# Optimization experiments

Measured on AMD Instinct MI355X. Metric: run time of the kernel, lower is better.

## Reference

```python
import jax, jax.numpy as jnp
import numpy as np

B, T, S, D, H = 4, 8, 512, 1024, 16
HD = D // H  # head dim = 64
N_LATENTS = 16


def setup_inputs() -> dict:
    key = jax.random.key(0)
    ks = jax.random.split(key, 10)
    x = jax.random.normal(ks[0], (B, T, S, D), dtype=jnp.float32)
    modality_ids = jax.random.randint(ks[1], (S,), 0, 8, dtype=jnp.int32)
    init = 0.02
    wq = jax.random.normal(ks[2], (D, H, HD), dtype=jnp.float32) * init
    wk = jax.random.normal(ks[3], (D, H, HD), dtype=jnp.float32) * init
    wv = jax.random.normal(ks[4], (D, H, HD), dtype=jnp.float32) * init
    wo = jax.random.normal(ks[5], (H, HD, D), dtype=jnp.float32) * init
    bq = jnp.zeros((H, HD), dtype=jnp.float32)
    bk = jnp.zeros((H, HD), dtype=jnp.float32)
    bv = jnp.zeros((H, HD), dtype=jnp.float32)
    bo = jnp.zeros((D,), dtype=jnp.float32)
    return {"x": x, "modality_ids": modality_ids, "wq": wq, "bq": bq,
            "wk": wk, "bk": bk, "wv": wv, "bv": bv, "wo": wo, "bo": bo}


def _encoder_mask(modality_ids, n_latents):
    # mask[q, k] = True means query q may attend to key k.
    # encoder mode: latent queries (index < n_latents) attend to everything,
    # non-latent queries attend only to same-modality keys.
    S_ = modality_ids.shape[0]
    is_q_lat = (jnp.arange(S_) < n_latents)[:, None]          # [S,1]
    same_mod = modality_ids[:, None] == modality_ids[None, :]  # [S,S]
    return jnp.where(is_q_lat, True, same_mod)                 # [S,S] bool


def reference(x, modality_ids, wq, bq, wk, bk, wv, bv, wo, bo):
    mask = _encoder_mask(modality_ids, N_LATENTS)  # [S,S]
    # QKV projections (flax DenseGeneral D -> (H, HD), with bias)
    q = jnp.einsum('btsd,dhc->btshc', x, wq) + bq
    k = jnp.einsum('btsd,dhc->btshc', x, wk) + bk
    v = jnp.einsum('btsd,dhc->btshc', x, wv) + bv
    # flax scales the query by 1/sqrt(head_dim) before the dot product
    q = q / jnp.sqrt(jnp.asarray(HD, dtype=q.dtype))
    scores = jnp.einsum('btqhc,btkhc->bthqk', q, k)  # [B,T,H,S,S]
    big_neg = jnp.finfo(scores.dtype).min
    scores = jnp.where(mask[None, None, None, :, :], scores, big_neg)
    attn = jax.nn.softmax(scores, axis=-1)
    out = jnp.einsum('bthqk,btkhc->btqhc', attn, v)  # [B,T,S,H,HD]
    y = jnp.einsum('btqhc,hcd->btqd', out, wo) + bo  # [B,T,S,D]
    return y
```

## Files before the change

### kernel.cpp

```cpp
#include <hip/hip_runtime.h>
#include <hip/hip_bf16.h>


typedef __attribute__((ext_vector_type(8))) short bf16x8;
typedef __attribute__((ext_vector_type(4))) float f32x4;
typedef __attribute__((ext_vector_type(16))) float f32x16;
typedef __attribute__((ext_vector_type(4))) unsigned short u16x4;
typedef __attribute__((ext_vector_type(2))) unsigned uint32x2;
typedef __attribute__((ext_vector_type(4))) unsigned uint32x4;

static __device__ __forceinline__ short f2bs(float f) {
  __hip_bfloat16 h = __float2bfloat16(f);
  return __builtin_bit_cast(short, h);
}

static __device__ __forceinline__ unsigned pack2bf(float a, float b) {
  return (unsigned)(unsigned short)f2bs(a) | ((unsigned)(unsigned short)f2bs(b) << 16);
}

static __device__ __forceinline__ void gload16(const void* g, void* l) {
  __builtin_amdgcn_global_load_lds(
      (const __attribute__((address_space(1))) void*)g,
      (__attribute__((address_space(3))) void*)l, 16, 0, 0);
}

__global__ __launch_bounds__(256) void cvt_x_kernel(const float* __restrict__ in,
                                                    __hip_bfloat16* __restrict__ out) {
  int i = blockIdx.x * 256 + threadIdx.x;
  const float4* p = (const float4*)in;
  float4 a = p[2 * i], b = p[2 * i + 1];
  bf16x8 v;
  v[0] = f2bs(a.x); v[1] = f2bs(a.y); v[2] = f2bs(a.z); v[3] = f2bs(a.w);
  v[4] = f2bs(b.x); v[5] = f2bs(b.y); v[6] = f2bs(b.z); v[7] = f2bs(b.w);
  *(bf16x8*)(out + (size_t)i * 8) = v;
}

__global__ __launch_bounds__(256) void trans_w_kernel(const float* __restrict__ in,
                                                      __hip_bfloat16* __restrict__ out) {
  __shared__ float tile[64][65];
  const int R0 = blockIdx.y * 64, C0 = blockIdx.x * 64;
  const int c = threadIdx.x & 63, r4 = threadIdx.x >> 6;
#pragma unroll
  for (int i = 0; i < 16; ++i) {
    int r = r4 * 16 + i;
    tile[r][c] = in[(size_t)(R0 + r) * 1024 + C0 + c];
  }
  __syncthreads();
#pragma unroll
  for (int i = 0; i < 16; ++i) {
    int r = r4 * 16 + i;
    out[(size_t)(C0 + r) * 1024 + R0 + c] = __float2bfloat16(tile[c][r]);
  }
}

template <int EPI>
__global__ __launch_bounds__(256) void gemm_bt(
    const __hip_bfloat16* __restrict__ A, const __hip_bfloat16* __restrict__ Bt,
    const float* __restrict__ bias0, const float* __restrict__ bias1,
    const float* __restrict__ bias2, __hip_bfloat16* __restrict__ o0,
    __hip_bfloat16* __restrict__ o1, __hip_bfloat16* __restrict__ o2,
    float* __restrict__ yout) {
  __shared__ __hip_bfloat16 Asm[128 * 64];
  __shared__ __hip_bfloat16 Bsm[128 * 64];
  const int tid = threadIdx.x;
  const int w = tid >> 6, lane = tid & 63;
  const int g = lane >> 4, l15 = lane & 15;
  const int wm = w >> 1, wn = w & 1;
  const long M0 = (long)blockIdx.y * 128, N0 = (long)blockIdx.x * 128;
  const int srow = lane >> 3;
  const int skk = (lane & 7) * 8;

  f32x4 acc[4][4];
  const f32x4 fz = {0.f, 0.f, 0.f, 0.f};
#pragma unroll
  for (int i = 0; i < 4; ++i)
#pragma unroll
    for (int j = 0; j < 4; ++j) acc[i][j] = fz;

  for (int kt = 0; kt < 16; ++kt) {
    const int k0 = kt * 64;
    __syncthreads();
#pragma unroll
    for (int i = 0; i < 4; ++i) {
      const int chunk = w * 4 + i;
      const int row = chunk * 8 + srow;
      gload16(A + (M0 + row) * 1024 + k0 + skk, Asm + chunk * 512);
      gload16(Bt + (N0 + row) * 1024 + k0 + skk, Bsm + chunk * 512);
    }
    __syncthreads();
#pragma unroll
    for (int ks = 0; ks < 2; ++ks) {
      bf16x8 af[4], bfr[4];
#pragma unroll
      for (int mt = 0; mt < 4; ++mt)
        af[mt] = *(const bf16x8*)(Asm + (wm * 64 + mt * 16 + l15) * 64 + ks * 32 + g * 8);
#pragma unroll
      for (int nt = 0; nt < 4; ++nt)
        bfr[nt] = *(const bf16x8*)(Bsm + (wn * 64 + nt * 16 + l15) * 64 + ks * 32 + g * 8);
#pragma unroll
      for (int mt = 0; mt < 4; ++mt)
#pragma unroll
        for (int nt = 0; nt < 4; ++nt)
          acc[mt][nt] = __builtin_amdgcn_mfma_f32_16x16x32_bf16(af[mt], bfr[nt],
                                                                acc[mt][nt], 0, 0, 0);
    }
  }

  const int mb = (int)M0 + wm * 64;
  const int nb = (int)N0 + wn * 64;
#pragma unroll
  for (int mt = 0; mt < 4; ++mt) {
    const int m0r = mb + mt * 16 + g * 4;
    const int bt_ = m0r >> 9, s0 = m0r & 511;
#pragma unroll
    for (int nt = 0; nt < 4; ++nt) {
      const int n = nb + nt * 16 + l15;
      f32x4 v = acc[mt][nt];
      if (EPI == 0) {
        const int t = n >> 10, r = n & 1023;
        const int h = r >> 6, c = r & 63;
        if (t == 0) {
          const float b = bias0[r];
          size_t base = (((size_t)bt_ * 16 + h) * 512 + s0) * 64 + c;
#pragma unroll
          for (int j = 0; j < 4; ++j)
            o0[base + (size_t)j * 64] = __float2bfloat16((v[j] + b) * 0.18033688f);
        } else if (t == 1) {
          const float b = bias1[r];
          size_t base = (((size_t)bt_ * 16 + h) * 512 + s0) * 64 + c;
#pragma unroll
          for (int j = 0; j < 4; ++j)
            o1[base + (size_t)j * 64] = __float2bfloat16(v[j] + b);
        } else {
          const float b = bias2[r];
          size_t base = (((size_t)bt_ * 16 + h) * 64 + c) * 512 + s0;
          u16x4 pk;
#pragma unroll
          for (int j = 0; j < 4; ++j) pk[j] = (unsigned short)f2bs(v[j] + b);
          *(u16x4*)(o2 + base) = pk;
        }
      } else {
        const float b = bias0[n];
        size_t base = (size_t)m0r * 1024 + n;
#pragma unroll
        for (int j = 0; j < 4; ++j) yout[base + (size_t)j * 1024] = v[j] + b;
      }
    }
  }
}

__global__ __launch_bounds__(256, 4) void attn_kernel(
    const __hip_bfloat16* __restrict__ Qb, const __hip_bfloat16* __restrict__ Kb,
    const __hip_bfloat16* __restrict__ Vt, const int* __restrict__ mids,
    __hip_bfloat16* __restrict__ Ao) {
  __shared__ unsigned char mids8[512];
  __shared__ float lbuf[4][32];
  const int tid = threadIdx.x;
  const int w = tid >> 6, lane = tid & 63;
  const int l31 = lane & 31, hi = lane >> 5;

  if (tid < 128) {
    const int4 mm = ((const int4*)mids)[tid];
    *(unsigned*)&mids8[tid * 4] = (mm.x & 255) | ((mm.y & 255) << 8) |
                                  ((mm.z & 255) << 16) | ((mm.w & 255) << 24);
  }

  const int bid = blockIdx.x;
  const int xcd = bid & 7, sl = bid >> 3;
  const int group = xcd * 64 + (sl >> 2);
  const int qb = sl & 3;
  const int h = group & 15, bt = group >> 4;

  const size_t hoff = ((size_t)bt * 16 + h) * 32768;
  const int qrow = qb * 128 + w * 32;

  bf16x8 qf[4];
#pragma unroll
  for (int s = 0; s < 4; ++s)
    qf[s] = *(const bf16x8*)(Qb + hoff + (size_t)(qrow + l31) * 64 + s * 16 + hi * 8);

  const int mq = mids[qrow + l31];
  const bool lat = (qrow + l31) < 16;
  float l_r = 0.f;
  f32x16 o0 = {0.f, 0.f, 0.f, 0.f, 0.f, 0.f, 0.f, 0.f,
               0.f, 0.f, 0.f, 0.f, 0.f, 0.f, 0.f, 0.f};
  f32x16 o1 = o0;

  __syncthreads();

  for (int kt = 0; kt < 16; ++kt) {
    const int kb = kt * 32;
    bf16x8 kf[4];
#pragma unroll
    for (int s = 0; s < 4; ++s)
      kf[s] = *(const bf16x8*)(Kb + hoff + (size_t)(kb + l31) * 64 + s * 16 + hi * 8);

    f32x16 sc = o0 * 0.f;
    __builtin_amdgcn_s_setprio(1);
#pragma unroll
    for (int s = 0; s < 4; ++s)
      sc = __builtin_amdgcn_mfma_f32_32x32x16_bf16(kf[s], qf[s], sc, 0, 0, 0);
    __builtin_amdgcn_s_setprio(0);

    bf16x8 vf[2][2];
#pragma unroll
    for (int s2 = 0; s2 < 2; ++s2)
#pragma unroll
      for (int ct = 0; ct < 2; ++ct)
        vf[s2][ct] = *(const bf16x8*)(Vt + hoff + (size_t)(ct * 32 + l31) * 512 + kb +
                                      s2 * 16 + hi * 8);

    unsigned mm[4];
#pragma unroll
    for (int m = 0; m < 4; ++m)
      mm[m] = *(const unsigned*)&mids8[kb + 4 * hi + 8 * m];
#pragma unroll
    for (int m = 0; m < 4; ++m)
#pragma unroll
      for (int j = 0; j < 4; ++j) {
        const int mk = (int)((mm[m] >> (8 * j)) & 255u);
        const bool valid = lat || (mk == mq);
        const float p = __builtin_amdgcn_exp2f(valid ? sc[4 * m + j] : -1e30f);
        sc[4 * m + j] = p;
        l_r += p;
      }

    bf16x8 pa[2];
#pragma unroll
    for (int s2 = 0; s2 < 2; ++s2) {
      const unsigned lo0 = pack2bf(sc[8 * s2 + 0], sc[8 * s2 + 1]);
      const unsigned lo1 = pack2bf(sc[8 * s2 + 2], sc[8 * s2 + 3]);
      const unsigned h0 = pack2bf(sc[8 * s2 + 4], sc[8 * s2 + 5]);
      const unsigned h1 = pack2bf(sc[8 * s2 + 6], sc[8 * s2 + 7]);
      const uint32x2 r0 = __builtin_amdgcn_permlane32_swap(lo0, h0, false, false);
      const uint32x2 r1 = __builtin_amdgcn_permlane32_swap(lo1, h1, false, false);
      const uint32x4 pw = {r0[0], r1[0], r0[1], r1[1]};
      pa[s2] = __builtin_bit_cast(bf16x8, pw);
    }

    __builtin_amdgcn_s_setprio(1);
    o0 = __builtin_amdgcn_mfma_f32_32x32x16_bf16(pa[0], vf[0][0], o0, 0, 0, 0);
    o1 = __builtin_amdgcn_mfma_f32_32x32x16_bf16(pa[0], vf[0][1], o1, 0, 0, 0);
    o0 = __builtin_amdgcn_mfma_f32_32x32x16_bf16(pa[1], vf[1][0], o0, 0, 0, 0);
    o1 = __builtin_amdgcn_mfma_f32_32x32x16_bf16(pa[1], vf[1][1], o1, 0, 0, 0);
    __builtin_amdgcn_s_setprio(0);
  }

  l_r += __shfl_xor(l_r, 32);
  if (hi == 0) lbuf[w][l31] = 1.0f / l_r;
  float4 lv[4];
#pragma unroll
  for (int m = 0; m < 4; ++m) lv[m] = *(const float4*)&lbuf[w][4 * hi + 8 * m];

#pragma unroll
  for (int m = 0; m < 4; ++m)
#pragma unroll
    for (int j = 0; j < 4; ++j) {
      const int ql = 4 * hi + 8 * m + j;
      const size_t base = ((size_t)bt * 512 + qrow + ql) * 1024 + h * 64 + l31;
      Ao[base] = __float2bfloat16(o0[4 * m + j] * lv[m][j]);
      Ao[base + 32] = __float2bfloat16(o1[4 * m + j] * lv[m][j]);
    }
}

extern "C" void kernel_launch(void* const* d_in, const int* in_sizes, int n_in,
                              void* d_out, int out_size, void* d_ws, size_t ws_size,
                              hipStream_t stream) {
  const float* x = (const float*)d_in[0];
  const int* mids = (const int*)d_in[1];
  const float* wq = (const float*)d_in[2];
  const float* bq = (const float*)d_in[3];
  const float* wk = (const float*)d_in[4];
  const float* bk = (const float*)d_in[5];
  const float* wv = (const float*)d_in[6];
  const float* bv = (const float*)d_in[7];
  const float* wo = (const float*)d_in[8];
  const float* bo = (const float*)d_in[9];
  float* y = (float*)d_out;

  char* ws = (char*)d_ws;
  __hip_bfloat16* xb  = (__hip_bfloat16*)(ws);
  __hip_bfloat16* wT  = (__hip_bfloat16*)(ws + 33554432);
  __hip_bfloat16* woT = (__hip_bfloat16*)(ws + 39845888);
  __hip_bfloat16* Qb  = (__hip_bfloat16*)(ws + 41943040);
  __hip_bfloat16* Kb  = (__hip_bfloat16*)(ws + 75497472);
  __hip_bfloat16* Vt  = (__hip_bfloat16*)(ws + 109051904);
  __hip_bfloat16* Ao  = xb;

  cvt_x_kernel<<<dim3(8192), dim3(256), 0, stream>>>(x, xb);
  trans_w_kernel<<<dim3(16, 16), dim3(256), 0, stream>>>(wq, wT);
  trans_w_kernel<<<dim3(16, 16), dim3(256), 0, stream>>>(wk, wT + 1048576);
  trans_w_kernel<<<dim3(16, 16), dim3(256), 0, stream>>>(wv, wT + 2097152);
  trans_w_kernel<<<dim3(16, 16), dim3(256), 0, stream>>>(wo, woT);

  gemm_bt<0><<<dim3(24, 128), dim3(256), 0, stream>>>(xb, wT, bq, bk, bv, Qb, Kb, Vt,
                                                      nullptr);
  attn_kernel<<<dim3(2048), dim3(256), 0, stream>>>(Qb, Kb, Vt, mids, Ao);
  gemm_bt<1><<<dim3(8, 128), dim3(256), 0, stream>>>(Ao, woT, bo, nullptr, nullptr,
                                                     nullptr, nullptr, nullptr, y);
}
```

Baseline: 486.1 us.

## Restructure GEMM into 256x256 tiles with multi-stage async LDS pipeline

Replaces the 128x128 single-buffered GEMM with a 512-thread kernel that computes 256x256 tiles. Each 64-wide K step is split into two 32-wide halves, and the LDS loads for the next two steps are prefetched asynchronously, with vmcnt waits in place of full syncthreads. It also remaps block IDs across XCDs for L2 locality and raises wave priority around the MFMA bursts. The goal is to hide global-load latency and get more operand reuse per tile, at the cost of 128KB of LDS per block (so low occupancy) and some wasted wrap-around prefetch loads on the last iterations.

```diff
diff --git a/kernel.cpp b/kernel.cpp
--- a/kernel.cpp
+++ b/kernel.cpp
@@ -53,79 +53,147 @@
   }
 }
 
+static __device__ __forceinline__ void stage_tile(
+    const __hip_bfloat16* __restrict__ src, long row0, int k0, char* lds_slot,
+    int w, int lane) {
+  const int r = lane >> 2, kc = (lane & 3) * 8;
+#pragma unroll
+  for (int i = 0; i < 2; ++i) {
+    const int row = (w * 2 + i) * 16 + r;
+    gload16(src + (row0 + row) * 1024 + k0 + kc, lds_slot + (w * 2 + i) * 1024);
+  }
+}
+
 template <int EPI>
-__global__ __launch_bounds__(256) void gemm_bt(
+__global__ __launch_bounds__(512, 2) void gemm_bt(
     const __hip_bfloat16* __restrict__ A, const __hip_bfloat16* __restrict__ Bt,
     const float* __restrict__ bias0, const float* __restrict__ bias1,
     const float* __restrict__ bias2, __hip_bfloat16* __restrict__ o0,
     __hip_bfloat16* __restrict__ o1, __hip_bfloat16* __restrict__ o2,
     float* __restrict__ yout) {
-  __shared__ __hip_bfloat16 Asm[128 * 64];
-  __shared__ __hip_bfloat16 Bsm[128 * 64];
+  __shared__ __align__(16) char ldsm[131072];
+#define ASLOT(tt, kh) (ldsm + ((((tt) & 1) * 2 + (kh)) << 14))
+#define BSLOT(tt, kh) (ldsm + 65536 + ((((tt) & 1) * 2 + (kh)) << 14))
   const int tid = threadIdx.x;
   const int w = tid >> 6, lane = tid & 63;
   const int g = lane >> 4, l15 = lane & 15;
-  const int wm = w >> 1, wn = w & 1;
-  const long M0 = (long)blockIdx.y * 128, N0 = (long)blockIdx.x * 128;
-  const int srow = lane >> 3;
-  const int skk = (lane & 7) * 8;
-
-  f32x4 acc[4][4];
+  const int wm = w >> 2, wn = w & 3;
+
+  const int nwg = (EPI == 0) ? 768 : 256;
+  const int wg = (blockIdx.x & 7) * (nwg >> 3) + (blockIdx.x >> 3);
+  const int by = wg & 63, bx = wg >> 6;
+  const long M0 = (long)by * 256, N0 = (long)bx * 256;
+
+  f32x4 acc[8][4];
   const f32x4 fz = {0.f, 0.f, 0.f, 0.f};
 #pragma unroll
-  for (int i = 0; i < 4; ++i)
+  for (int i = 0; i < 8; ++i)
 #pragma unroll
     for (int j = 0; j < 4; ++j) acc[i][j] = fz;
 
-  for (int kt = 0; kt < 16; ++kt) {
-    const int k0 = kt * 64;
-    __syncthreads();
-#pragma unroll
-    for (int i = 0; i < 4; ++i) {
-      const int chunk = w * 4 + i;
-      const int row = chunk * 8 + srow;
-      gload16(A + (M0 + row) * 1024 + k0 + skk, Asm + chunk * 512);
-      gload16(Bt + (N0 + row) * 1024 + k0 + skk, Bsm + chunk * 512);
-    }
-    __syncthreads();
-#pragma unroll
-    for (int ks = 0; ks < 2; ++ks) {
-      bf16x8 af[4], bfr[4];
-#pragma unroll
-      for (int mt = 0; mt < 4; ++mt)
-        af[mt] = *(const bf16x8*)(Asm + (wm * 64 + mt * 16 + l15) * 64 + ks * 32 + g * 8);
+  stage_tile(A, M0, 0, ASLOT(0, 0), w, lane);
+  stage_tile(Bt, N0, 0, BSLOT(0, 0), w, lane);
+  stage_tile(A, M0, 32, ASLOT(0, 1), w, lane);
+  stage_tile(Bt, N0, 32, BSLOT(0, 1), w, lane);
+  stage_tile(A, M0, 64, ASLOT(1, 0), w, lane);
+  stage_tile(Bt, N0, 64, BSLOT(1, 0), w, lane);
+
+  for (int t = 0; t < 16; ++t) {
+    const int kN1 = ((t + 1) & 15) * 64;
+    const int kN2 = ((t + 2) & 15) * 64;
+    bf16x8 bk[4], af[4];
+
+    asm volatile("s_waitcnt vmcnt(8)" ::: "memory");
+    __builtin_amdgcn_s_barrier();
+    __builtin_amdgcn_sched_barrier(0);
+    stage_tile(A, M0, kN1 + 32, ASLOT(t + 1, 1), w, lane);
+    {
+      const char* as0 = ASLOT(t, 0);
+      const char* bs0 = BSLOT(t, 0);
 #pragma unroll
       for (int nt = 0; nt < 4; ++nt)
-        bfr[nt] = *(const bf16x8*)(Bsm + (wn * 64 + nt * 16 + l15) * 64 + ks * 32 + g * 8);
+        bk[nt] = *(const bf16x8*)(bs0 + (wn * 64 + nt * 16 + l15) * 64 + g * 16);
+#pragma unroll
+      for (int mt = 0; mt < 4; ++mt)
+        af[mt] = *(const bf16x8*)(as0 + (wm * 128 + mt * 16 + l15) * 64 + g * 16);
+      __builtin_amdgcn_s_setprio(1);
 #pragma unroll
       for (int mt = 0; mt < 4; ++mt)
 #pragma unroll
         for (int nt = 0; nt < 4; ++nt)
-          acc[mt][nt] = __builtin_amdgcn_mfma_f32_16x16x32_bf16(af[mt], bfr[nt],
+          acc[mt][nt] = __builtin_amdgcn_mfma_f32_16x16x32_bf16(af[mt], bk[nt],
                                                                 acc[mt][nt], 0, 0, 0);
-    }
-  }
-
-  const int mb = (int)M0 + wm * 64;
-  const int nb = (int)N0 + wn * 64;
-#pragma unroll
-  for (int mt = 0; mt < 4; ++mt) {
-    const int m0r = mb + mt * 16 + g * 4;
+      __builtin_amdgcn_s_setprio(0);
+
+      stage_tile(Bt, N0, kN1 + 32, BSLOT(t + 1, 1), w, lane);
+#pragma unroll
+      for (int mt = 0; mt < 4; ++mt)
+        af[mt] = *(const bf16x8*)(as0 + (wm * 128 + 64 + mt * 16 + l15) * 64 + g * 16);
+      __builtin_amdgcn_s_setprio(1);
+#pragma unroll
+      for (int mt = 0; mt < 4; ++mt)
+#pragma unroll
+        for (int nt = 0; nt < 4; ++nt)
+          acc[4 + mt][nt] = __builtin_amdgcn_mfma_f32_16x16x32_bf16(
+              af[mt], bk[nt], acc[4 + mt][nt], 0, 0, 0);
+      __builtin_amdgcn_s_setprio(0);
+    }
+
+    asm volatile("s_waitcnt vmcnt(8)" ::: "memory");
+    __builtin_amdgcn_s_barrier();
+    __builtin_amdgcn_sched_barrier(0);
+    stage_tile(A, M0, kN2, ASLOT(t + 2, 0), w, lane);
+    {
+      const char* as1 = ASLOT(t, 1);
+      const char* bs1 = BSLOT(t, 1);
+#pragma unroll
+      for (int nt = 0; nt < 4; ++nt)
+        bk[nt] = *(const bf16x8*)(bs1 + (wn * 64 + nt * 16 + l15) * 64 + g * 16);
+#pragma unroll
+      for (int mt = 0; mt < 4; ++mt)
+        af[mt] = *(const bf16x8*)(as1 + (wm * 128 + mt * 16 + l15) * 64 + g * 16);
+      __builtin_amdgcn_s_setprio(1);
+#pragma unroll
+      for (int mt = 0; mt < 4; ++mt)
+#pragma unroll
+        for (int nt = 0; nt < 4; ++nt)
+          acc[mt][nt] = __builtin_amdgcn_mfma_f32_16x16x32_bf16(af[mt], bk[nt],
+                                                                acc[mt][nt], 0, 0, 0);
+      __builtin_amdgcn_s_setprio(0);
+
+      stage_tile(Bt, N0, kN2, BSLOT(t + 2, 0), w, lane);
+#pragma unroll
+      for (int mt = 0; mt < 4; ++mt)
+        af[mt] = *(const bf16x8*)(as1 + (wm * 128 + 64 + mt * 16 + l15) * 64 + g * 16);
+      __builtin_amdgcn_s_setprio(1);
+#pragma unroll
+      for (int mt = 0; mt < 4; ++mt)
+#pragma unroll
+        for (int nt = 0; nt < 4; ++nt)
+          acc[4 + mt][nt] = __builtin_amdgcn_mfma_f32_16x16x32_bf16(
+              af[mt], bk[nt], acc[4 + mt][nt], 0, 0, 0);
+      __builtin_amdgcn_s_setprio(0);
+    }
+  }
+
+#pragma unroll
+  for (int mt = 0; mt < 8; ++mt) {
+    const int m0r = (int)M0 + wm * 128 + mt * 16 + g * 4;
     const int bt_ = m0r >> 9, s0 = m0r & 511;
 #pragma unroll
     for (int nt = 0; nt < 4; ++nt) {
-      const int n = nb + nt * 16 + l15;
+      const int n = (int)N0 + wn * 64 + nt * 16 + l15;
       f32x4 v = acc[mt][nt];
       if (EPI == 0) {
-        const int t = n >> 10, r = n & 1023;
+        const int tq = n >> 10, r = n & 1023;
         const int h = r >> 6, c = r & 63;
-        if (t == 0) {
+        if (tq == 0) {
           const float b = bias0[r];
           size_t base = (((size_t)bt_ * 16 + h) * 512 + s0) * 64 + c;
 #pragma unroll
           for (int j = 0; j < 4; ++j)
             o0[base + (size_t)j * 64] = __float2bfloat16((v[j] + b) * 0.18033688f);
-        } else if (t == 1) {
+        } else if (tq == 1) {
           const float b = bias1[r];
           size_t base = (((size_t)bt_ * 16 + h) * 512 + s0) * 64 + c;
 #pragma unroll
@@ -147,6 +215,8 @@
       }
     }
   }
+#undef ASLOT
+#undef BSLOT
 }
 
 __global__ __launch_bounds__(256, 4) void attn_kernel(
@@ -293,9 +363,9 @@
   trans_w_kernel<<<dim3(16, 16), dim3(256), 0, stream>>>(wv, wT + 2097152);
   trans_w_kernel<<<dim3(16, 16), dim3(256), 0, stream>>>(wo, woT);
 
-  gemm_bt<0><<<dim3(24, 128), dim3(256), 0, stream>>>(xb, wT, bq, bk, bv, Qb, Kb, Vt,
-                                                      nullptr);
+  gemm_bt<0><<<dim3(768), dim3(512), 0, stream>>>(xb, wT, bq, bk, bv, Qb, Kb, Vt,
+                                                  nullptr);
   attn_kernel<<<dim3(2048), dim3(256), 0, stream>>>(Qb, Kb, Vt, mids, Ao);
-  gemm_bt<1><<<dim3(8, 128), dim3(256), 0, stream>>>(Ao, woT, bo, nullptr, nullptr,
-                                                     nullptr, nullptr, nullptr, y);
-}
+  gemm_bt<1><<<dim3(256), dim3(512), 0, stream>>>(Ao, woT, bo, nullptr, nullptr,
+                                                  nullptr, nullptr, nullptr, y);
+}
```

After: 447.6 us. -7.9%, faster.
